# Performance work log

Hardware: AMD Instinct MI355X
Metric: run time of the kernel (lower is better)

The kernel has to match this reference:

```python
import jax, jax.numpy as jnp
import numpy as np

EMB = 1024
HEADS = 16

def setup_inputs() -> dict:
    key = jax.random.key(0)
    ks = jax.random.split(key, 9)
    s = 1.0 / np.sqrt(EMB)
    return {
        "x": jax.random.normal(ks[0], (2, 2048, EMB), dtype=jnp.float32),
        "Wq": jax.random.normal(ks[1], (EMB, EMB), dtype=jnp.float32) * s,
        "bq": jnp.zeros((EMB,), dtype=jnp.float32),
        "Wk": jax.random.normal(ks[2], (EMB, EMB), dtype=jnp.float32) * s,
        "bk": jnp.zeros((EMB,), dtype=jnp.float32),
        "Wv": jax.random.normal(ks[3], (EMB, EMB), dtype=jnp.float32) * s,
        "bv": jnp.zeros((EMB,), dtype=jnp.float32),
        "Wo": jax.random.normal(ks[4], (EMB, EMB), dtype=jnp.float32) * s,
        "bo": jnp.zeros((EMB,), dtype=jnp.float32),
    }

def reference(x, Wq, bq, Wk, bk, Wv, bv, Wo, bo):
    b, n, e = x.shape
    h = HEADS
    d = e // h
    def split_heads(t):
        return t.reshape(b, n, h, d).transpose(0, 2, 1, 3)  # b h n d
    q = split_heads(x @ Wq + bq)
    k = split_heads(x @ Wk + bk)
    v = split_heads(x @ Wv + bv)
    scores = jnp.einsum('bhqd,bhkd->bhqk', q, k)
    # NOTE: original module applies softmax FIRST, then divides by sqrt(emb_size)
    attn = jax.nn.softmax(scores, axis=-1) / jnp.sqrt(jnp.float32(e))
    out = jnp.einsum('bhqk,bhkd->bhqd', attn, v)
    out = out.transpose(0, 2, 1, 3).reshape(b, n, e)
    return out @ Wo + bo
```

## Files before the change

### kernel.cpp

```cpp
#include <hip/hip_runtime.h>
#include <hip/hip_bf16.h>

#define B_ 2
#define N_ 2048
#define E_ 1024
#define H_ 16
#define D_ 64
#define T_ (B_*N_)

using s16x8 = __attribute__((ext_vector_type(8))) short;
using f32x4 = __attribute__((ext_vector_type(4))) float;

static __device__ __forceinline__ short f2bf(float f) {
    __hip_bfloat16 h = __float2bfloat16(f);
    union { __hip_bfloat16 h; short s; } u; u.h = h; return u.s;
}
static __device__ __forceinline__ float bf2f(short s) {
    union { short s; __hip_bfloat16 h; } u; u.s = s;
    return __bfloat162float(u.h);
}

typedef const __attribute__((address_space(1))) unsigned int gas_u32;
typedef __attribute__((address_space(3))) unsigned int las_u32;
static __device__ __forceinline__ void gl_lds16(const void* g, void* l) {
    __builtin_amdgcn_global_load_lds((gas_u32*)g, (las_u32*)l, 16, 0, 0);
}

__global__ __launch_bounds__(256)
void split_x_k(const float* __restrict__ x, short* __restrict__ xh, short* __restrict__ xl)
{
    const int total = (T_*E_)/4;
    for (int i = blockIdx.x*256 + threadIdx.x; i < total; i += gridDim.x*256) {
        const float4 v = ((const float4*)x)[i];
        short h0 = f2bf(v.x), h1 = f2bf(v.y), h2 = f2bf(v.z), h3 = f2bf(v.w);
        short l0 = f2bf(v.x - bf2f(h0)), l1 = f2bf(v.y - bf2f(h1));
        short l2 = f2bf(v.z - bf2f(h2)), l3 = f2bf(v.w - bf2f(h3));
        short4 hs; hs.x=h0; hs.y=h1; hs.z=h2; hs.w=h3;
        short4 ls; ls.x=l0; ls.y=l1; ls.z=l2; ls.w=l3;
        ((short4*)xh)[i] = hs;
        ((short4*)xl)[i] = ls;
    }
}

template<int SPLIT>
__global__ __launch_bounds__(256)
void splitwT_k(const float* __restrict__ W, short* __restrict__ WhT, short* __restrict__ WlT)
{
    __shared__ float Ts[64][65];
    const int t = threadIdx.x;
    const int kb = blockIdx.x*64, nb = blockIdx.y*64;
    const int r = t>>4, c4 = (t&15)*4;
    #pragma unroll
    for (int l = 0; l < 4; ++l) {
        const float4 v = *(const float4*)&W[(size_t)(kb + r + l*16)*E_ + nb + c4];
        Ts[c4+0][r+l*16] = v.x; Ts[c4+1][r+l*16] = v.y;
        Ts[c4+2][r+l*16] = v.z; Ts[c4+3][r+l*16] = v.w;
    }
    __syncthreads();
    #pragma unroll
    for (int l = 0; l < 4; ++l) {
        const int np = r + l*16;
        float v0 = Ts[np][c4+0], v1 = Ts[np][c4+1], v2 = Ts[np][c4+2], v3 = Ts[np][c4+3];
        short4 hs; hs.x=f2bf(v0); hs.y=f2bf(v1); hs.z=f2bf(v2); hs.w=f2bf(v3);
        *(short4*)&WhT[(size_t)(nb + np)*E_ + kb + c4] = hs;
        if (SPLIT) {
            short4 ls;
            ls.x = f2bf(v0 - bf2f(hs.x)); ls.y = f2bf(v1 - bf2f(hs.y));
            ls.z = f2bf(v2 - bf2f(hs.z)); ls.w = f2bf(v3 - bf2f(hs.w));
            *(short4*)&WlT[(size_t)(nb + np)*E_ + kb + c4] = ls;
        }
    }
}

template<int NPROD, int EPI>
__global__ __launch_bounds__(256)
void gemm_mfma_k(const short* __restrict__ Ah_g, const short* __restrict__ Al_g,
                 const short* __restrict__ Bh_g, const short* __restrict__ Bl_g,
                 const float* __restrict__ bias, void* __restrict__ out0,
                 void* __restrict__ out1)
{
    __shared__ __align__(16) short Ah[2][64*64];
    __shared__ __align__(16) short Bh[2][128*64];

    const int lane = threadIdx.x & 63, wid = threadIdx.x >> 6;
    const int lr = lane & 15, lg = lane >> 4;
    const int bm = blockIdx.x >> 3, bn = blockIdx.x & 7;
    const int wm = (wid>>1)*32, wn = (wid&1)*64;
    const int gm0 = bm*64 + wm;
    const int gn0 = bn*128 + wn;

    const int lrow = lane >> 3;
    const int lsw8 = (((lane & 7) ^ lrow)) * 8;

    f32x4 acc[2][4];
    #pragma unroll
    for (int i = 0; i < 2; ++i)
        #pragma unroll
        for (int j = 0; j < 4; ++j)
            acc[i][j] = (f32x4){0.f,0.f,0.f,0.f};

    #pragma unroll
    for (int s = 0; s < 6; ++s) {
        const int j = wid + 4*s;
        if (j < 8)
            gl_lds16(Ah_g + (size_t)(bm*64 + j*8 + lrow)*E_ + lsw8, &Ah[0][j*512]);
        else
            gl_lds16(Bh_g + (size_t)(bn*128 + (j-8)*8 + lrow)*E_ + lsw8, &Bh[0][(j-8)*512]);
    }
    __syncthreads();

    for (int t = 0; t < 16; ++t) {
        const int cur = t & 1;
        const int k0  = t*64;
        if (t < 15) {
            const int kn = k0 + 64;
            #pragma unroll
            for (int s = 0; s < 6; ++s) {
                const int j = wid + 4*s;
                if (j < 8)
                    gl_lds16(Ah_g + (size_t)(bm*64 + j*8 + lrow)*E_ + kn + lsw8, &Ah[cur^1][j*512]);
                else
                    gl_lds16(Bh_g + (size_t)(bn*128 + (j-8)*8 + lrow)*E_ + kn + lsw8, &Bh[cur^1][(j-8)*512]);
            }
        }
        s16x8 a1[2][2], b1[2][4];
        if (NPROD == 3) {
            #pragma unroll
            for (int kc = 0; kc < 2; ++kc) {
                #pragma unroll
                for (int mi = 0; mi < 2; ++mi)
                    a1[kc][mi] = *(const s16x8*)(Al_g + (size_t)(gm0 + mi*16 + lr)*E_ + k0 + kc*32 + lg*8);
                #pragma unroll
                for (int ni = 0; ni < 4; ++ni)
                    b1[kc][ni] = *(const s16x8*)(Bl_g + (size_t)(gn0 + ni*16 + lr)*E_ + k0 + kc*32 + lg*8);
            }
        }
        #pragma unroll
        for (int kc = 0; kc < 2; ++kc) {
            s16x8 a0[2], b0[4];
            #pragma unroll
            for (int mi = 0; mi < 2; ++mi) {
                const int ar = wm + mi*16 + lr;
                a0[mi] = *(const s16x8*)&Ah[cur][ar*64 + (((kc*4+lg) ^ (ar&7))<<3)];
            }
            #pragma unroll
            for (int ni = 0; ni < 4; ++ni) {
                const int br = wn + ni*16 + lr;
                b0[ni] = *(const s16x8*)&Bh[cur][br*64 + (((kc*4+lg) ^ (br&7))<<3)];
            }
            #pragma unroll
            for (int mi = 0; mi < 2; ++mi)
                #pragma unroll
                for (int ni = 0; ni < 4; ++ni) {
                    acc[mi][ni] = __builtin_amdgcn_mfma_f32_16x16x32_bf16(a0[mi], b0[ni], acc[mi][ni], 0, 0, 0);
                    if (NPROD == 3) {
                        acc[mi][ni] = __builtin_amdgcn_mfma_f32_16x16x32_bf16(a0[mi], b1[kc][ni], acc[mi][ni], 0, 0, 0);
                        acc[mi][ni] = __builtin_amdgcn_mfma_f32_16x16x32_bf16(a1[kc][mi], b0[ni], acc[mi][ni], 0, 0, 0);
                    }
                }
        }
        __syncthreads();
    }

    #pragma unroll
    for (int mi = 0; mi < 2; ++mi)
        #pragma unroll
        for (int ni = 0; ni < 4; ++ni) {
            const int gn = gn0 + ni*16 + lr;
            const float bv = bias[gn];
            if (EPI == 0) {
                float* out = (float*)out0;
                #pragma unroll
                for (int r = 0; r < 4; ++r) {
                    const int row = gm0 + mi*16 + lg*4 + r;
                    out[(size_t)row*E_ + gn] = acc[mi][ni][r] + bv;
                }
            } else if (EPI == 1) {
                short* oh = (short*)out0; short* ol = (short*)out1;
                const int h = gn >> 6, d = gn & 63;
                #pragma unroll
                for (int r = 0; r < 4; ++r) {
                    const int row = gm0 + mi*16 + lg*4 + r;
                    const int b = row >> 11, n = row & (N_-1);
                    const size_t idx = (((size_t)(b*H_ + h))*N_ + n)*D_ + d;
                    const float v = acc[mi][ni][r] + bv;
                    const short hi = f2bf(v);
                    oh[idx] = hi;
                    ol[idx] = f2bf(v - bf2f(hi));
                }
            } else {
                short* ov = (short*)out0;
                const int h = gn >> 6, d = gn & 63;
                const int row0 = gm0 + mi*16 + lg*4;
                const int b = row0 >> 11, n0 = row0 & (N_-1);
                short4 s4;
                s4.x = f2bf(acc[mi][ni][0] + bv);
                s4.y = f2bf(acc[mi][ni][1] + bv);
                s4.z = f2bf(acc[mi][ni][2] + bv);
                s4.w = f2bf(acc[mi][ni][3] + bv);
                *(short4*)&ov[(((size_t)(b*H_ + h))*D_ + d)*N_ + n0] = s4;
            }
        }
}

__global__ __launch_bounds__(256)
void attn_mfma_k(const short* __restrict__ qh, const short* __restrict__ ql,
                 const short* __restrict__ kh, const short* __restrict__ kl,
                 const short* __restrict__ vT, short* __restrict__ aO)
{
    __shared__ __align__(16) short Khs[2][64*64];
    __shared__ __align__(16) short Vts[2][64*64];
    __shared__ __align__(16) short P[128][72];

    const int i = blockIdx.x;
    const int xcd = i & 7, j = i >> 3;
    const int bh = xcd*4 + (j >> 4);
    const int q0 = (j & 15) * 128;

    const int lane = threadIdx.x & 63, wid = threadIdx.x >> 6;
    const int lr = lane & 15, lg = lane >> 4;
    const int wq = wid * 32;

    const short* qhb = qh + (size_t)bh*N_*D_;
    const short* qlb = ql + (size_t)bh*N_*D_;
    const short* khb = kh + (size_t)bh*N_*D_;
    const short* klb = kl + (size_t)bh*N_*D_;
    const short* vb  = vT + (size_t)bh*D_*N_;

    const int lrow = lane >> 3;
    const int lsw8 = (((lane & 7) ^ lrow)) * 8;

    s16x8 q0f[2][2], q1f[2][2];
    #pragma unroll
    for (int mi = 0; mi < 2; ++mi)
        #pragma unroll
        for (int kc = 0; kc < 2; ++kc) {
            const size_t off = (size_t)(q0 + wq + mi*16 + lr)*D_ + kc*32 + lg*8;
            q0f[mi][kc] = *(const s16x8*)(qhb + off);
            q1f[mi][kc] = *(const s16x8*)(qlb + off);
        }

    f32x4 o[2][4];
    float lp[2][4];
    #pragma unroll
    for (int mi = 0; mi < 2; ++mi) {
        #pragma unroll
        for (int ni = 0; ni < 4; ++ni) o[mi][ni] = (f32x4){0.f,0.f,0.f,0.f};
        #pragma unroll
        for (int r = 0; r < 4; ++r) lp[mi][r] = 0.f;
    }

    #pragma unroll
    for (int s = 0; s < 4; ++s) {
        const int jj = wid + 4*s;
        if (jj < 8)
            gl_lds16(khb + (size_t)(jj*8 + lrow)*D_ + lsw8, &Khs[0][jj*512]);
        else
            gl_lds16(vb + (size_t)((jj-8)*8 + lrow)*N_ + lsw8, &Vts[0][(jj-8)*512]);
    }
    __syncthreads();

    for (int t = 0; t < 32; ++t) {
        const int cur = t & 1;
        const int kv0 = t*64;
        if (t < 31) {
            const int kvn = kv0 + 64;
            #pragma unroll
            for (int s = 0; s < 4; ++s) {
                const int jj = wid + 4*s;
                if (jj < 8)
                    gl_lds16(khb + (size_t)(kvn + jj*8 + lrow)*D_ + lsw8, &Khs[cur^1][jj*512]);
                else
                    gl_lds16(vb + (size_t)((jj-8)*8 + lrow)*N_ + kvn + lsw8, &Vts[cur^1][(jj-8)*512]);
            }
        }
        s16x8 klv[2][4];
        #pragma unroll
        for (int kc = 0; kc < 2; ++kc)
            #pragma unroll
            for (int ni = 0; ni < 4; ++ni)
                klv[kc][ni] = *(const s16x8*)(klb + (size_t)(kv0 + ni*16 + lr)*D_ + kc*32 + lg*8);

        f32x4 s[2][4];
        #pragma unroll
        for (int mi = 0; mi < 2; ++mi)
            #pragma unroll
            for (int ni = 0; ni < 4; ++ni) s[mi][ni] = (f32x4){0.f,0.f,0.f,0.f};

        #pragma unroll
        for (int kc = 0; kc < 2; ++kc)
            #pragma unroll
            for (int ni = 0; ni < 4; ++ni) {
                const int kr = ni*16 + lr;
                const s16x8 kh8 = *(const s16x8*)&Khs[cur][kr*64 + (((kc*4+lg) ^ (kr&7))<<3)];
                #pragma unroll
                for (int mi = 0; mi < 2; ++mi) {
                    s[mi][ni] = __builtin_amdgcn_mfma_f32_16x16x32_bf16(q0f[mi][kc], kh8, s[mi][ni], 0, 0, 0);
                    s[mi][ni] = __builtin_amdgcn_mfma_f32_16x16x32_bf16(q0f[mi][kc], klv[kc][ni], s[mi][ni], 0, 0, 0);
                    s[mi][ni] = __builtin_amdgcn_mfma_f32_16x16x32_bf16(q1f[mi][kc], kh8, s[mi][ni], 0, 0, 0);
                }
            }

        #pragma unroll
        for (int mi = 0; mi < 2; ++mi)
            #pragma unroll
            for (int r = 0; r < 4; ++r) {
                float acc_l = 0.f;
                #pragma unroll
                for (int ni = 0; ni < 4; ++ni) {
                    const float p = __expf(s[mi][ni][r]);
                    s[mi][ni][r] = p;
                    acc_l += p;
                }
                lp[mi][r] += acc_l;
            }

        #pragma unroll
        for (int mi = 0; mi < 2; ++mi)
            #pragma unroll
            for (int ni = 0; ni < 4; ++ni)
                #pragma unroll
                for (int r = 0; r < 4; ++r)
                    P[wq + mi*16 + lg*4 + r][ni*16 + lr] = f2bf(s[mi][ni][r]);

        #pragma unroll
        for (int kc = 0; kc < 2; ++kc) {
            s16x8 p8[2];
            #pragma unroll
            for (int mi = 0; mi < 2; ++mi)
                p8[mi] = *(const s16x8*)&P[wq + mi*16 + lr][kc*32 + lg*8];
            #pragma unroll
            for (int ni = 0; ni < 4; ++ni) {
                const int vr = ni*16 + lr;
                const s16x8 v8 = *(const s16x8*)&Vts[cur][vr*64 + (((kc*4+lg) ^ (vr&7))<<3)];
                #pragma unroll
                for (int mi = 0; mi < 2; ++mi)
                    o[mi][ni] = __builtin_amdgcn_mfma_f32_16x16x32_bf16(p8[mi], v8, o[mi][ni], 0, 0, 0);
            }
        }
        __syncthreads();
    }

    const int b = bh >> 4, h = bh & 15;
    #pragma unroll
    for (int mi = 0; mi < 2; ++mi)
        #pragma unroll
        for (int r = 0; r < 4; ++r) {
            float l = lp[mi][r];
            l += __shfl_xor(l, 1);
            l += __shfl_xor(l, 2);
            l += __shfl_xor(l, 4);
            l += __shfl_xor(l, 8);
            const float inv = 1.0f / (l * 32.0f);
            const int n = q0 + wq + mi*16 + lg*4 + r;
            #pragma unroll
            for (int ni = 0; ni < 4; ++ni) {
                const int e = h*64 + ni*16 + lr;
                aO[(size_t)(b*N_ + n)*E_ + e] = f2bf(o[mi][ni][r] * inv);
            }
        }
}

extern "C" void kernel_launch(void* const* d_in, const int* in_sizes, int n_in,
                              void* d_out, int out_size, void* d_ws, size_t ws_size,
                              hipStream_t stream)
{
    const float* x  = (const float*)d_in[0];
    const float* Wq = (const float*)d_in[1];
    const float* bq = (const float*)d_in[2];
    const float* Wk = (const float*)d_in[3];
    const float* bk = (const float*)d_in[4];
    const float* Wv = (const float*)d_in[5];
    const float* bv = (const float*)d_in[6];
    const float* Wo = (const float*)d_in[7];
    const float* bo = (const float*)d_in[8];
    float* out = (float*)d_out;

    const size_t MB = 1024*1024ULL;
    char* ws = (char*)d_ws;
    short* xh  = (short*)(ws + 0*MB);
    short* xl  = (short*)(ws + 8*MB);
    short* WhT = (short*)(ws + 16*MB);
    short* WlT = (short*)(ws + 18*MB);
    short* vT  = (short*)(ws + 20*MB);
    short* qh  = (short*)(ws + 28*MB);
    short* ql  = (short*)(ws + 36*MB);
    short* kh  = (short*)(ws + 44*MB);
    short* kl  = (short*)(ws + 52*MB);
    short* aO  = (short*)(ws + 0*MB);

    dim3 gw(16, 16);

    split_x_k<<<1024, 256, 0, stream>>>(x, xh, xl);

    splitwT_k<0><<<gw, 256, 0, stream>>>(Wv, WhT, nullptr);
    gemm_mfma_k<1,2><<<512, 256, 0, stream>>>(xh, nullptr, WhT, nullptr, bv, vT, nullptr);

    splitwT_k<1><<<gw, 256, 0, stream>>>(Wq, WhT, WlT);
    gemm_mfma_k<3,1><<<512, 256, 0, stream>>>(xh, xl, WhT, WlT, bq, qh, ql);

    splitwT_k<1><<<gw, 256, 0, stream>>>(Wk, WhT, WlT);
    gemm_mfma_k<3,1><<<512, 256, 0, stream>>>(xh, xl, WhT, WlT, bk, kh, kl);

    attn_mfma_k<<<512, 256, 0, stream>>>(qh, ql, kh, kl, vT, aO);

    splitwT_k<0><<<gw, 256, 0, stream>>>(Wo, WhT, nullptr);
    gemm_mfma_k<1,0><<<512, 256, 0, stream>>>(aO, nullptr, WhT, nullptr, bo, out, nullptr);
}
```

Measured before the change: 354.5 us.

## Stage low-part GEMM operands in LDS and halve attention query tile per block

In the GEMM kernel, the low-precision halves of A and B are now staged through shared memory alongside the high halves instead of being read per-lane straight from global memory. The double-buffered prefetch is dropped for a single buffer with a sync after each load. The attention kernel now gives each block 64 query rows instead of 128, one 16-row tile per wave, and launches twice as many blocks. This trades K/V reuse per block for more parallelism and less register pressure, and the loss of load/compute overlap in the GEMM may cost time.

```diff
diff --git a/kernel.cpp b/kernel.cpp
--- a/kernel.cpp
+++ b/kernel.cpp
@@ -79,8 +79,10 @@
                  const float* __restrict__ bias, void* __restrict__ out0,
                  void* __restrict__ out1)
 {
-    __shared__ __align__(16) short Ah[2][64*64];
-    __shared__ __align__(16) short Bh[2][128*64];
+    __shared__ __align__(16) short Ah[64*64];
+    __shared__ __align__(16) short Bh[128*64];
+    __shared__ __align__(16) short Al[(NPROD==3)?64*64:8];
+    __shared__ __align__(16) short Bl[(NPROD==3)?128*64:8];
 
     const int lane = threadIdx.x & 63, wid = threadIdx.x >> 6;
     const int lr = lane & 15, lg = lane >> 4;
@@ -99,54 +101,48 @@
         for (int j = 0; j < 4; ++j)
             acc[i][j] = (f32x4){0.f,0.f,0.f,0.f};
 
-    #pragma unroll
-    for (int s = 0; s < 6; ++s) {
-        const int j = wid + 4*s;
-        if (j < 8)
-            gl_lds16(Ah_g + (size_t)(bm*64 + j*8 + lrow)*E_ + lsw8, &Ah[0][j*512]);
-        else
-            gl_lds16(Bh_g + (size_t)(bn*128 + (j-8)*8 + lrow)*E_ + lsw8, &Bh[0][(j-8)*512]);
-    }
-    __syncthreads();
-
-    for (int t = 0; t < 16; ++t) {
-        const int cur = t & 1;
-        const int k0  = t*64;
-        if (t < 15) {
-            const int kn = k0 + 64;
+    for (int k0 = 0; k0 < E_; k0 += 64) {
+        if (NPROD == 3) {
+            #pragma unroll
+            for (int s = 0; s < 12; ++s) {
+                const int j = wid + 4*s;
+                if (j < 8)
+                    gl_lds16(Ah_g + (size_t)(bm*64 + j*8 + lrow)*E_ + k0 + lsw8, &Ah[j*512]);
+                else if (j < 16)
+                    gl_lds16(Al_g + (size_t)(bm*64 + (j-8)*8 + lrow)*E_ + k0 + lsw8, &Al[(j-8)*512]);
+                else if (j < 32)
+                    gl_lds16(Bh_g + (size_t)(bn*128 + (j-16)*8 + lrow)*E_ + k0 + lsw8, &Bh[(j-16)*512]);
+                else
+                    gl_lds16(Bl_g + (size_t)(bn*128 + (j-32)*8 + lrow)*E_ + k0 + lsw8, &Bl[(j-32)*512]);
+            }
+        } else {
             #pragma unroll
             for (int s = 0; s < 6; ++s) {
                 const int j = wid + 4*s;
                 if (j < 8)
-                    gl_lds16(Ah_g + (size_t)(bm*64 + j*8 + lrow)*E_ + kn + lsw8, &Ah[cur^1][j*512]);
+                    gl_lds16(Ah_g + (size_t)(bm*64 + j*8 + lrow)*E_ + k0 + lsw8, &Ah[j*512]);
                 else
-                    gl_lds16(Bh_g + (size_t)(bn*128 + (j-8)*8 + lrow)*E_ + kn + lsw8, &Bh[cur^1][(j-8)*512]);
-            }
-        }
-        s16x8 a1[2][2], b1[2][4];
-        if (NPROD == 3) {
-            #pragma unroll
-            for (int kc = 0; kc < 2; ++kc) {
-                #pragma unroll
-                for (int mi = 0; mi < 2; ++mi)
-                    a1[kc][mi] = *(const s16x8*)(Al_g + (size_t)(gm0 + mi*16 + lr)*E_ + k0 + kc*32 + lg*8);
-                #pragma unroll
-                for (int ni = 0; ni < 4; ++ni)
-                    b1[kc][ni] = *(const s16x8*)(Bl_g + (size_t)(gn0 + ni*16 + lr)*E_ + k0 + kc*32 + lg*8);
-            }
-        }
+                    gl_lds16(Bh_g + (size_t)(bn*128 + (j-8)*8 + lrow)*E_ + k0 + lsw8, &Bh[(j-8)*512]);
+            }
+        }
+        __syncthreads();
+
         #pragma unroll
         for (int kc = 0; kc < 2; ++kc) {
-            s16x8 a0[2], b0[4];
+            s16x8 a0[2], a1[2], b0[4], b1[4];
             #pragma unroll
             for (int mi = 0; mi < 2; ++mi) {
                 const int ar = wm + mi*16 + lr;
-                a0[mi] = *(const s16x8*)&Ah[cur][ar*64 + (((kc*4+lg) ^ (ar&7))<<3)];
+                const int ao = ar*64 + (((kc*4+lg) ^ (ar&7))<<3);
+                a0[mi] = *(const s16x8*)&Ah[ao];
+                if (NPROD == 3) a1[mi] = *(const s16x8*)&Al[ao];
             }
             #pragma unroll
             for (int ni = 0; ni < 4; ++ni) {
                 const int br = wn + ni*16 + lr;
-                b0[ni] = *(const s16x8*)&Bh[cur][br*64 + (((kc*4+lg) ^ (br&7))<<3)];
+                const int bo = br*64 + (((kc*4+lg) ^ (br&7))<<3);
+                b0[ni] = *(const s16x8*)&Bh[bo];
+                if (NPROD == 3) b1[ni] = *(const s16x8*)&Bl[bo];
             }
             #pragma unroll
             for (int mi = 0; mi < 2; ++mi)
@@ -154,8 +150,8 @@
                 for (int ni = 0; ni < 4; ++ni) {
                     acc[mi][ni] = __builtin_amdgcn_mfma_f32_16x16x32_bf16(a0[mi], b0[ni], acc[mi][ni], 0, 0, 0);
                     if (NPROD == 3) {
-                        acc[mi][ni] = __builtin_amdgcn_mfma_f32_16x16x32_bf16(a0[mi], b1[kc][ni], acc[mi][ni], 0, 0, 0);
-                        acc[mi][ni] = __builtin_amdgcn_mfma_f32_16x16x32_bf16(a1[kc][mi], b0[ni], acc[mi][ni], 0, 0, 0);
+                        acc[mi][ni] = __builtin_amdgcn_mfma_f32_16x16x32_bf16(a0[mi], b1[ni], acc[mi][ni], 0, 0, 0);
+                        acc[mi][ni] = __builtin_amdgcn_mfma_f32_16x16x32_bf16(a1[mi], b0[ni], acc[mi][ni], 0, 0, 0);
                     }
                 }
         }
@@ -210,16 +206,16 @@
 {
     __shared__ __align__(16) short Khs[2][64*64];
     __shared__ __align__(16) short Vts[2][64*64];
-    __shared__ __align__(16) short P[128][72];
+    __shared__ __align__(16) short P[64][72];
 
     const int i = blockIdx.x;
     const int xcd = i & 7, j = i >> 3;
-    const int bh = xcd*4 + (j >> 4);
-    const int q0 = (j & 15) * 128;
+    const int bh = xcd*4 + (j >> 5);
+    const int q0 = (j & 31) * 64;
 
     const int lane = threadIdx.x & 63, wid = threadIdx.x >> 6;
     const int lr = lane & 15, lg = lane >> 4;
-    const int wq = wid * 32;
+    const int wq = wid * 16;
 
     const short* qhb = qh + (size_t)bh*N_*D_;
     const short* qlb = ql + (size_t)bh*N_*D_;
@@ -230,25 +226,20 @@
     const int lrow = lane >> 3;
     const int lsw8 = (((lane & 7) ^ lrow)) * 8;
 
-    s16x8 q0f[2][2], q1f[2][2];
-    #pragma unroll
-    for (int mi = 0; mi < 2; ++mi)
-        #pragma unroll
-        for (int kc = 0; kc < 2; ++kc) {
-            const size_t off = (size_t)(q0 + wq + mi*16 + lr)*D_ + kc*32 + lg*8;
-            q0f[mi][kc] = *(const s16x8*)(qhb + off);
-            q1f[mi][kc] = *(const s16x8*)(qlb + off);
-        }
-
-    f32x4 o[2][4];
-    float lp[2][4];
-    #pragma unroll
-    for (int mi = 0; mi < 2; ++mi) {
-        #pragma unroll
-        for (int ni = 0; ni < 4; ++ni) o[mi][ni] = (f32x4){0.f,0.f,0.f,0.f};
-        #pragma unroll
-        for (int r = 0; r < 4; ++r) lp[mi][r] = 0.f;
-    }
+    s16x8 q0f[2], q1f[2];
+    #pragma unroll
+    for (int kc = 0; kc < 2; ++kc) {
+        const size_t off = (size_t)(q0 + wq + lr)*D_ + kc*32 + lg*8;
+        q0f[kc] = *(const s16x8*)(qhb + off);
+        q1f[kc] = *(const s16x8*)(qlb + off);
+    }
+
+    f32x4 o[4];
+    float lp[4];
+    #pragma unroll
+    for (int ni = 0; ni < 4; ++ni) o[ni] = (f32x4){0.f,0.f,0.f,0.f};
+    #pragma unroll
+    for (int r = 0; r < 4; ++r) lp[r] = 0.f;
 
     #pragma unroll
     for (int s = 0; s < 4; ++s) {
@@ -263,6 +254,13 @@
     for (int t = 0; t < 32; ++t) {
         const int cur = t & 1;
         const int kv0 = t*64;
+        s16x8 klv[2][4];
+        #pragma unroll
+        for (int kc = 0; kc < 2; ++kc)
+            #pragma unroll
+            for (int ni = 0; ni < 4; ++ni)
+                klv[kc][ni] = *(const s16x8*)(klb + (size_t)(kv0 + ni*16 + lr)*D_ + kc*32 + lg*8);
+
         if (t < 31) {
             const int kvn = kv0 + 64;
             #pragma unroll
@@ -274,68 +272,54 @@
                     gl_lds16(vb + (size_t)((jj-8)*8 + lrow)*N_ + kvn + lsw8, &Vts[cur^1][(jj-8)*512]);
             }
         }
-        s16x8 klv[2][4];
+
+        f32x4 s[4];
+        #pragma unroll
+        for (int ni = 0; ni < 4; ++ni) s[ni] = (f32x4){0.f,0.f,0.f,0.f};
+
+        s16x8 kh8[2][4];
         #pragma unroll
         for (int kc = 0; kc < 2; ++kc)
             #pragma unroll
-            for (int ni = 0; ni < 4; ++ni)
-                klv[kc][ni] = *(const s16x8*)(klb + (size_t)(kv0 + ni*16 + lr)*D_ + kc*32 + lg*8);
-
-        f32x4 s[2][4];
-        #pragma unroll
-        for (int mi = 0; mi < 2; ++mi)
-            #pragma unroll
-            for (int ni = 0; ni < 4; ++ni) s[mi][ni] = (f32x4){0.f,0.f,0.f,0.f};
-
+            for (int ni = 0; ni < 4; ++ni) {
+                const int kr = ni*16 + lr;
+                kh8[kc][ni] = *(const s16x8*)&Khs[cur][kr*64 + (((kc*4+lg) ^ (kr&7))<<3)];
+                s[ni] = __builtin_amdgcn_mfma_f32_16x16x32_bf16(q0f[kc], kh8[kc][ni], s[ni], 0, 0, 0);
+            }
         #pragma unroll
         for (int kc = 0; kc < 2; ++kc)
             #pragma unroll
             for (int ni = 0; ni < 4; ++ni) {
-                const int kr = ni*16 + lr;
-                const s16x8 kh8 = *(const s16x8*)&Khs[cur][kr*64 + (((kc*4+lg) ^ (kr&7))<<3)];
-                #pragma unroll
-                for (int mi = 0; mi < 2; ++mi) {
-                    s[mi][ni] = __builtin_amdgcn_mfma_f32_16x16x32_bf16(q0f[mi][kc], kh8, s[mi][ni], 0, 0, 0);
-                    s[mi][ni] = __builtin_amdgcn_mfma_f32_16x16x32_bf16(q0f[mi][kc], klv[kc][ni], s[mi][ni], 0, 0, 0);
-                    s[mi][ni] = __builtin_amdgcn_mfma_f32_16x16x32_bf16(q1f[mi][kc], kh8, s[mi][ni], 0, 0, 0);
-                }
-            }
-
-        #pragma unroll
-        for (int mi = 0; mi < 2; ++mi)
-            #pragma unroll
-            for (int r = 0; r < 4; ++r) {
-                float acc_l = 0.f;
-                #pragma unroll
-                for (int ni = 0; ni < 4; ++ni) {
-                    const float p = __expf(s[mi][ni][r]);
-                    s[mi][ni][r] = p;
-                    acc_l += p;
-                }
-                lp[mi][r] += acc_l;
-            }
-
-        #pragma unroll
-        for (int mi = 0; mi < 2; ++mi)
-            #pragma unroll
-            for (int ni = 0; ni < 4; ++ni)
-                #pragma unroll
-                for (int r = 0; r < 4; ++r)
-                    P[wq + mi*16 + lg*4 + r][ni*16 + lr] = f2bf(s[mi][ni][r]);
+                s[ni] = __builtin_amdgcn_mfma_f32_16x16x32_bf16(q0f[kc], klv[kc][ni], s[ni], 0, 0, 0);
+                s[ni] = __builtin_amdgcn_mfma_f32_16x16x32_bf16(q1f[kc], kh8[kc][ni], s[ni], 0, 0, 0);
+            }
+
+        #pragma unroll
+        for (int r = 0; r < 4; ++r) {
+            float acc_l = 0.f;
+            #pragma unroll
+            for (int ni = 0; ni < 4; ++ni) {
+                const float p = __expf(s[ni][r]);
+                s[ni][r] = p;
+                acc_l += p;
+            }
+            lp[r] += acc_l;
+        }
+
+        #pragma unroll
+        for (int ni = 0; ni < 4; ++ni)
+            #pragma unroll
+            for (int r = 0; r < 4; ++r)
+                P[wq + lg*4 + r][ni*16 + lr] = f2bf(s[ni][r]);
 
         #pragma unroll
         for (int kc = 0; kc < 2; ++kc) {
-            s16x8 p8[2];
-            #pragma unroll
-            for (int mi = 0; mi < 2; ++mi)
-                p8[mi] = *(const s16x8*)&P[wq + mi*16 + lr][kc*32 + lg*8];
+            const s16x8 p8 = *(const s16x8*)&P[wq + lr][kc*32 + lg*8];
             #pragma unroll
             for (int ni = 0; ni < 4; ++ni) {
                 const int vr = ni*16 + lr;
                 const s16x8 v8 = *(const s16x8*)&Vts[cur][vr*64 + (((kc*4+lg) ^ (vr&7))<<3)];
-                #pragma unroll
-                for (int mi = 0; mi < 2; ++mi)
-                    o[mi][ni] = __builtin_amdgcn_mfma_f32_16x16x32_bf16(p8[mi], v8, o[mi][ni], 0, 0, 0);
+                o[ni] = __builtin_amdgcn_mfma_f32_16x16x32_bf16(p8, v8, o[ni], 0, 0, 0);
             }
         }
         __syncthreads();
@@ -343,22 +327,20 @@
 
     const int b = bh >> 4, h = bh & 15;
     #pragma unroll
-    for (int mi = 0; mi < 2; ++mi)
-        #pragma unroll
-        for (int r = 0; r < 4; ++r) {
-            float l = lp[mi][r];
-            l += __shfl_xor(l, 1);
-            l += __shfl_xor(l, 2);
-            l += __shfl_xor(l, 4);
-            l += __shfl_xor(l, 8);
-            const float inv = 1.0f / (l * 32.0f);
-            const int n = q0 + wq + mi*16 + lg*4 + r;
-            #pragma unroll
-            for (int ni = 0; ni < 4; ++ni) {
-                const int e = h*64 + ni*16 + lr;
-                aO[(size_t)(b*N_ + n)*E_ + e] = f2bf(o[mi][ni][r] * inv);
-            }
-        }
+    for (int r = 0; r < 4; ++r) {
+        float l = lp[r];
+        l += __shfl_xor(l, 1);
+        l += __shfl_xor(l, 2);
+        l += __shfl_xor(l, 4);
+        l += __shfl_xor(l, 8);
+        const float inv = 1.0f / (l * 32.0f);
+        const int n = q0 + wq + lg*4 + r;
+        #pragma unroll
+        for (int ni = 0; ni < 4; ++ni) {
+            const int e = h*64 + ni*16 + lr;
+            aO[(size_t)(b*N_ + n)*E_ + e] = f2bf(o[ni][r] * inv);
+        }
+    }
 }
 
 extern "C" void kernel_launch(void* const* d_in, const int* in_sizes, int n_in,
@@ -402,7 +384,7 @@
     splitwT_k<1><<<gw, 256, 0, stream>>>(Wk, WhT, WlT);
     gemm_mfma_k<3,1><<<512, 256, 0, stream>>>(xh, xl, WhT, WlT, bk, kh, kl);
 
-    attn_mfma_k<<<512, 256, 0, stream>>>(qh, ql, kh, kl, vT, aO);
+    attn_mfma_k<<<1024, 256, 0, stream>>>(qh, ql, kh, kl, vT, aO);
 
     splitwT_k<0><<<gw, 256, 0, stream>>>(Wo, WhT, nullptr);
     gemm_mfma_k<1,0><<<512, 256, 0, stream>>>(aO, nullptr, WhT, nullptr, bo, out, nullptr);
```

After: 360.1 us. Within noise of the previous version (+1.6%).
